# Optimization experiments

Hardware: AMD Instinct MI355X
Metric: run time of the kernel (lower is better)

## Reference

```python
import jax, jax.numpy as jnp
import numpy as np

N_NODES = 100000
N_EDGES = 1600000
N_IN = 8
N_PRE = 32
C = 128
N_LAYERS = 8


def _lin(key, fan_in, fan_out):
    kw, kb = jax.random.split(key)
    s = 1.0 / np.sqrt(fan_in).astype(np.float32)
    W = jax.random.uniform(kw, (fan_in, fan_out), minval=-s, maxval=s, dtype=jnp.float32)
    b = jax.random.uniform(kb, (fan_out,), minval=-s, maxval=s, dtype=jnp.float32)
    return W, b


def setup_inputs() -> dict:
    key = jax.random.key(0)
    ks = jax.random.split(key, 9)
    x = jax.random.normal(ks[0], (N_NODES, N_IN), dtype=jnp.float32)
    edge_index = jax.random.randint(ks[1], (2, N_EDGES), 0, N_NODES, dtype=jnp.int32)
    Wp, bp = _lin(ks[2], N_IN, N_PRE)      # preproc
    W1, b1 = _lin(ks[3], N_PRE, C)         # fc_input_1 (node_identity)
    W2, b2 = _lin(ks[4], N_PRE, C)         # fc_input_2
    Wg, bg = _lin(ks[5], C, C)             # tied GCNConv weight/bias
    Wd, bd = _lin(ks[6], 2 * C, C)         # tied dense fusion
    Wf1, bf1 = _lin(ks[7], 2 * C, C)       # final_fc1
    Wf2, bf2 = _lin(ks[8], C, 2)           # final_fc2
    return {"x": x, "edge_index": edge_index, "Wp": Wp, "bp": bp, "W1": W1, "b1": b1,
            "W2": W2, "b2": b2, "Wg": Wg, "bg": bg, "Wd": Wd, "bd": bd,
            "Wf1": Wf1, "bf1": bf1, "Wf2": Wf2, "bf2": bf2}


def _gcn(h, Wg, bg, src, dst):
    # PyG GCNConv: add self-loops, norm = deg^-1/2[src] * deg^-1/2[dst].
    # Norm factorizes, so scale at node level instead of per edge.
    hw = h @ Wg                                                  # [N, C]
    deg = jnp.zeros((N_NODES,), jnp.float32).at[dst].add(1.0) + 1.0  # +1 self-loop
    dis = jax.lax.rsqrt(deg)                                     # deg^-1/2
    hs = hw * dis[:, None]
    agg = jax.ops.segment_sum(hs[src], dst, num_segments=N_NODES)
    return (agg + hs) * dis[:, None] + bg                        # hs term = self-loop (deg^-1 * hw)


def reference(x, edge_index, Wp, bp, W1, b1, W2, b2, Wg, bg, Wd, bd, Wf1, bf1, Wf2, bf2):
    src, dst = edge_index[0], edge_index[1]
    h0 = x @ Wp + bp                       # preproc_activation = none
    ni = jax.nn.relu(h0 @ W1 + b1)         # node_identity
    h = jax.nn.relu(h0 @ W2 + b2)
    for _ in range(N_LAYERS):              # tied gnn layers; dropout is identity (inference)
        g = jax.nn.relu(_gcn(h, Wg, bg, src, dst))
        h = jax.nn.relu(jnp.concatenate([ni, g], axis=1) @ Wd + bd)
    h = jax.nn.relu(jnp.concatenate([ni, h], axis=1) @ Wf1 + bf1)
    return h @ Wf2 + bf2                   # output_activation never applied in forward
```

## Files before the change

kernel.cpp:

```cpp
#include <hip/hip_runtime.h>

#define N_NODES 100000
#define N_EDGES 1600000
#define NB 391
#define NTASK (N_NODES / 16)
#define COLPAD (N_EDGES + 7 * N_NODES + 64)

typedef unsigned short ushort_t;
typedef __attribute__((ext_vector_type(8))) short bf16x8;
typedef __attribute__((ext_vector_type(4))) float f32x4;

__device__ __forceinline__ float bf2f(unsigned short u) {
    union { unsigned u; float f; } x; x.u = ((unsigned)u) << 16; return x.f;
}
__device__ __forceinline__ unsigned short f2bf(float f) {
    union { float f; unsigned u; } x; x.f = f;
    unsigned r = x.u + 0x7fffu + ((x.u >> 16) & 1u);
    return (unsigned short)(r >> 16);
}

__global__ void k_zero(unsigned* p, int n) {
    int i = blockIdx.x * 256 + threadIdx.x;
    if (i < n) p[i] = 0u;
}

__global__ void k_filld(unsigned* p) {
    int i = blockIdx.x * 256 + threadIdx.x;
    if (i < COLPAD) p[i] = (unsigned)N_NODES;
}

__global__ void k_deg(const int* __restrict__ dst, unsigned* __restrict__ cnt) {
    int e = blockIdx.x * 256 + threadIdx.x;
    if (e < N_EDGES) atomicAdd(&cnt[dst[e]], 1u);
}

__global__ void k_dis(const unsigned* __restrict__ cnt, float* __restrict__ dis,
                      float* __restrict__ sdeg) {
    int i = blockIdx.x * 256 + threadIdx.x;
    if (i < N_NODES) {
        float d = (float)cnt[i] + 1.0f;
        float s = sqrtf(d);
        sdeg[i] = s;
        dis[i] = 1.0f / s;
    }
}

__global__ void __launch_bounds__(256) k_bsum(const unsigned* __restrict__ cnt,
                                              unsigned* __restrict__ bsum) {
    __shared__ unsigned sh[256];
    int i = blockIdx.x * 256 + threadIdx.x;
    sh[threadIdx.x] = (i < N_NODES) ? ((cnt[i] + 7u) & ~7u) : 0u;
    __syncthreads();
    for (int off = 128; off > 0; off >>= 1) {
        if (threadIdx.x < off) sh[threadIdx.x] += sh[threadIdx.x + off];
        __syncthreads();
    }
    if (threadIdx.x == 0) bsum[blockIdx.x] = sh[0];
}

__global__ void __launch_bounds__(512) k_bscan(unsigned* __restrict__ bsum) {
    __shared__ unsigned sh[512];
    int t = threadIdx.x;
    unsigned v = (t < NB) ? bsum[t] : 0u;
    sh[t] = v;
    __syncthreads();
    for (int off = 1; off < 512; off <<= 1) {
        unsigned u = (t >= off) ? sh[t - off] : 0u;
        __syncthreads();
        sh[t] += u;
        __syncthreads();
    }
    if (t < NB) bsum[t] = sh[t] - v;
}

__global__ void __launch_bounds__(256) k_apply(const unsigned* __restrict__ cnt,
                                               const unsigned* __restrict__ bsum,
                                               unsigned* __restrict__ prow,
                                               unsigned* __restrict__ cur) {
    __shared__ unsigned sh[256];
    int i = blockIdx.x * 256 + threadIdx.x;
    int t = threadIdx.x;
    unsigned v = (i < N_NODES) ? ((cnt[i] + 7u) & ~7u) : 0u;
    sh[t] = v;
    __syncthreads();
    for (int off = 1; off < 256; off <<= 1) {
        unsigned u = (t >= off) ? sh[t - off] : 0u;
        __syncthreads();
        sh[t] += u;
        __syncthreads();
    }
    if (i < N_NODES) {
        prow[i] = bsum[blockIdx.x] + sh[t] - v;
        cur[i] = 0u;
    }
    if (i == N_NODES - 1) prow[N_NODES] = bsum[blockIdx.x] + sh[t];
}

__global__ void k_fill(const int* __restrict__ src, const int* __restrict__ dst,
                       const unsigned* __restrict__ prow, unsigned* __restrict__ cur,
                       unsigned* __restrict__ colp) {
    int e = blockIdx.x * 256 + threadIdx.x;
    if (e < N_EDGES) {
        int d = dst[e];
        unsigned pos = prow[d] + atomicAdd(&cur[d], 1u);
        colp[pos] = (unsigned)src[e];
    }
}

__global__ void k_dummy(ushort_t* hdA, ushort_t* hdB) {
    int t = threadIdx.x;
    if (t < 128) hdA[(size_t)N_NODES * 128 + t] = 0;
    else hdB[(size_t)N_NODES * 128 + (t - 128)] = 0;
}

__global__ void k_tr(const float* __restrict__ Wd, const float* __restrict__ Wf1,
                     const float* __restrict__ Wg, ushort_t* __restrict__ WT) {
    const float* srcs[5] = {Wd, Wf1, Wg, Wd + 128 * 128, Wf1 + 128 * 128};
    const float* S = srcs[blockIdx.x];
    ushort_t* Dhi = WT + (size_t)(2 * blockIdx.x) * 16384;
    ushort_t* Dlo = Dhi + 16384;
    for (int i = threadIdx.x; i < 128 * 128; i += blockDim.x) {
        int n = i >> 7, k = i & 127;
        float w = S[k * 128 + n];
        unsigned short h = f2bf(w);
        Dhi[n * 128 + k] = h;
        Dlo[n * 128 + k] = f2bf(w - bf2f(h));
    }
}

__global__ void __launch_bounds__(128) k_pre1(
    const float* __restrict__ x, const float* __restrict__ Wp,
    const float* __restrict__ bp, const float* __restrict__ W1,
    const float* __restrict__ b1, const float* __restrict__ W2,
    const float* __restrict__ b2, const float* __restrict__ dis,
    ushort_t* __restrict__ ni, ushort_t* __restrict__ hd) {
    __shared__ float h0s[4][32];
    int j = threadIdx.x;
    long n0 = (long)blockIdx.x * 4;
    {
        int nn = j >> 5, c = j & 31;
        float acc = bp[c];
#pragma unroll
        for (int k = 0; k < 8; ++k)
            acc += x[(n0 + nn) * 8 + k] * Wp[k * 32 + c];
        h0s[nn][c] = acc;
    }
    __syncthreads();
    float ni_a[4], h1_a[4];
    float bb1 = b1[j], bb2 = b2[j];
#pragma unroll
    for (int m = 0; m < 4; ++m) { ni_a[m] = bb1; h1_a[m] = bb2; }
    for (int cc = 0; cc < 32; ++cc) {
        float w1 = W1[cc * 128 + j];
        float w2 = W2[cc * 128 + j];
#pragma unroll
        for (int m = 0; m < 4; ++m) {
            float h0v = h0s[m][cc];
            ni_a[m] += h0v * w1;
            h1_a[m] += h0v * w2;
        }
    }
#pragma unroll
    for (int m = 0; m < 4; ++m) {
        long node = n0 + m;
        ni[node * 128 + j] = f2bf(fmaxf(ni_a[m], 0.f));
        hd[node * 128 + j] = f2bf(fmaxf(h1_a[m], 0.f) * dis[node]);
    }
}

__device__ __forceinline__ void load_split_frags(const float* __restrict__ p,
                                                 bf16x8* ahi, bf16x8* alo) {
#pragma unroll
    for (int kc = 0; kc < 4; ++kc) {
        const float* q = p + kc * 32;
#pragma unroll
        for (int j = 0; j < 8; ++j) {
            float f = q[j];
            unsigned short h = f2bf(f);
            ahi[kc][j] = (short)h;
            alo[kc][j] = (short)f2bf(f - bf2f(h));
        }
    }
}

__device__ __forceinline__ void mfma_tiles(const bf16x8* ahi, const bf16x8* alo,
                                           const ushort_t* __restrict__ WThi,
                                           const ushort_t* __restrict__ WTlo,
                                           int r16, int q, f32x4* acc) {
#pragma unroll
    for (int t = 0; t < 8; ++t) {
        const ushort_t* bh = WThi + (t * 16 + r16) * 128 + q * 8;
        const ushort_t* bl = WTlo + (t * 16 + r16) * 128 + q * 8;
#pragma unroll
        for (int kc = 0; kc < 4; ++kc) {
            bf16x8 bhv = *(const bf16x8*)(bh + kc * 32);
            bf16x8 blv = *(const bf16x8*)(bl + kc * 32);
            acc[t] = __builtin_amdgcn_mfma_f32_16x16x32_bf16(alo[kc], bhv, acc[t], 0, 0, 0);
            acc[t] = __builtin_amdgcn_mfma_f32_16x16x32_bf16(ahi[kc], blv, acc[t], 0, 0, 0);
            acc[t] = __builtin_amdgcn_mfma_f32_16x16x32_bf16(ahi[kc], bhv, acc[t], 0, 0, 0);
        }
    }
}

__global__ void __launch_bounds__(256) gemm_bias(
    const ushort_t* __restrict__ in, const ushort_t* __restrict__ WThi,
    const ushort_t* __restrict__ WTlo, const float* __restrict__ bias,
    ushort_t* __restrict__ out) {
    int task = blockIdx.x * 4 + (threadIdx.x >> 6);
    if (task >= NTASK) return;
    int lane = threadIdx.x & 63;
    int q = lane >> 4, r16 = lane & 15;
    long base = (long)task * 16;

    bf16x8 a[4];
    const ushort_t* arow = in + (base + r16) * 128 + q * 8;
#pragma unroll
    for (int kc = 0; kc < 4; ++kc) a[kc] = *(const bf16x8*)(arow + kc * 32);

    f32x4 acc[8];
#pragma unroll
    for (int t = 0; t < 8; ++t) acc[t] = {0.f, 0.f, 0.f, 0.f};
#pragma unroll
    for (int t = 0; t < 8; ++t) {
        const ushort_t* bh = WThi + (t * 16 + r16) * 128 + q * 8;
        const ushort_t* bl = WTlo + (t * 16 + r16) * 128 + q * 8;
#pragma unroll
        for (int kc = 0; kc < 4; ++kc) {
            bf16x8 bhv = *(const bf16x8*)(bh + kc * 32);
            bf16x8 blv = *(const bf16x8*)(bl + kc * 32);
            acc[t] = __builtin_amdgcn_mfma_f32_16x16x32_bf16(a[kc], blv, acc[t], 0, 0, 0);
            acc[t] = __builtin_amdgcn_mfma_f32_16x16x32_bf16(a[kc], bhv, acc[t], 0, 0, 0);
        }
    }
#pragma unroll
    for (int t = 0; t < 8; ++t) {
        int n = t * 16 + r16;
        float bv = bias[n];
#pragma unroll
        for (int r = 0; r < 4; ++r) {
            long node = base + q * 4 + r;
            out[node * 128 + n] = f2bf(acc[t][r] + bv);
        }
    }
}

__device__ __forceinline__ void acc8(uint4 w, float* a) {
    a[0] += __uint_as_float(w.x << 16);
    a[1] += __uint_as_float(w.x & 0xffff0000u);
    a[2] += __uint_as_float(w.y << 16);
    a[3] += __uint_as_float(w.y & 0xffff0000u);
    a[4] += __uint_as_float(w.z << 16);
    a[5] += __uint_as_float(w.z & 0xffff0000u);
    a[6] += __uint_as_float(w.w << 16);
    a[7] += __uint_as_float(w.w & 0xffff0000u);
}

__device__ __forceinline__ void gather8(uint4* G, uint4 c0, uint4 c1,
                                        const uint4* __restrict__ h4, int l) {
    G[0] = h4[(long)c0.x * 16 + l];
    G[1] = h4[(long)c0.y * 16 + l];
    G[2] = h4[(long)c0.z * 16 + l];
    G[3] = h4[(long)c0.w * 16 + l];
    G[4] = h4[(long)c1.x * 16 + l];
    G[5] = h4[(long)c1.y * 16 + l];
    G[6] = h4[(long)c1.z * 16 + l];
    G[7] = h4[(long)c1.w * 16 + l];
}

__device__ __forceinline__ void accbatch(const uint4* G, float* a) {
#pragma unroll
    for (int j = 0; j < 8; ++j) acc8(G[j], a);
}

__global__ void __launch_bounds__(256, 3) k_fused(
    const unsigned* __restrict__ prow, const unsigned* __restrict__ colp,
    const ushort_t* __restrict__ hd_in,
    const ushort_t* __restrict__ hi_wg, const ushort_t* __restrict__ lo_wg,
    const float* __restrict__ bg,
    const ushort_t* __restrict__ hi_wd, const ushort_t* __restrict__ lo_wd,
    const ushort_t* __restrict__ niWd, const float* __restrict__ dis,
    ushort_t* __restrict__ hd_out) {
    __shared__ float gsh[4][16 * 132];
    int wid = threadIdx.x >> 6;
    int lane = threadIdx.x & 63;
    int task = blockIdx.x * 4 + wid;
    if (task >= NTASK) return;
    long base = (long)task * 16;
    float* gw = gsh[wid];
    const uint4* h4 = (const uint4*)hd_in;

    int g = lane >> 4;
    int l = lane & 15;

#pragma unroll 1
    for (int i = 0; i < 4; ++i) {
        int m = g * 4 + i;
        long node = base + m;
        float a[8] = {0.f, 0.f, 0.f, 0.f, 0.f, 0.f, 0.f, 0.f};
        uint4 own = h4[node * 16 + l];
        unsigned t0 = prow[node];
        int nb = (int)((prow[node + 1] - t0) >> 3);
        acc8(own, a);
        if (nb > 0) {
            const uint4* cp = (const uint4*)(colp + t0);
            uint4 cX0 = cp[0], cX1 = cp[1];
            uint4 cY0 = cp[2], cY1 = cp[3];
            cp += 4;
            uint4 GA[8], GB[8];
            gather8(GA, cX0, cX1, h4, l);
            int k = 0;
            for (; k + 2 < nb; k += 2) {
                cX0 = cp[0]; cX1 = cp[1];
                gather8(GB, cY0, cY1, h4, l);
                accbatch(GA, a);
                cY0 = cp[2]; cY1 = cp[3];
                cp += 4;
                gather8(GA, cX0, cX1, h4, l);
                accbatch(GB, a);
            }
            if (nb - k == 2) {
                gather8(GB, cY0, cY1, h4, l);
                accbatch(GA, a);
                accbatch(GB, a);
            } else {
                accbatch(GA, a);
            }
        }
        float* dstp = gw + m * 132 + 8 * l;
        *(float4*)dstp = make_float4(a[0], a[1], a[2], a[3]);
        *(float4*)(dstp + 4) = make_float4(a[4], a[5], a[6], a[7]);
    }

    int q = lane >> 4, r16 = lane & 15;
    bf16x8 ahi[4], alo[4];
    load_split_frags(gw + r16 * 132 + q * 8, ahi, alo);

    f32x4 acc[8];
#pragma unroll
    for (int t = 0; t < 8; ++t) acc[t] = {0.f, 0.f, 0.f, 0.f};
    mfma_tiles(ahi, alo, hi_wg, lo_wg, r16, q, acc);

    float sc[4];
#pragma unroll
    for (int r = 0; r < 4; ++r) sc[r] = dis[base + q * 4 + r];

#pragma unroll
    for (int t = 0; t < 8; ++t) {
        int n = t * 16 + r16;
        float bv = bg[n];
#pragma unroll
        for (int r = 0; r < 4; ++r) {
            int m = q * 4 + r;
            gw[m * 132 + n] = fmaxf(acc[t][r] * sc[r] + bv, 0.f);
        }
    }

    load_split_frags(gw + r16 * 132 + q * 8, ahi, alo);
#pragma unroll
    for (int t = 0; t < 8; ++t) acc[t] = {0.f, 0.f, 0.f, 0.f};
    mfma_tiles(ahi, alo, hi_wd, lo_wd, r16, q, acc);

#pragma unroll
    for (int t = 0; t < 8; ++t) {
        int n = t * 16 + r16;
#pragma unroll
        for (int r = 0; r < 4; ++r) {
            long node = base + q * 4 + r;
            float nv = bf2f(niWd[node * 128 + n]);
            hd_out[node * 128 + n] = f2bf(fmaxf(acc[t][r] + nv, 0.f) * sc[r]);
        }
    }
}

__global__ void __launch_bounds__(256) k_fin(
    const ushort_t* __restrict__ in, const ushort_t* __restrict__ WThi,
    const ushort_t* __restrict__ WTlo, const ushort_t* __restrict__ niWf,
    const float* __restrict__ sdeg, float* __restrict__ out) {
    int task = blockIdx.x * 4 + (threadIdx.x >> 6);
    if (task >= NTASK) return;
    int lane = threadIdx.x & 63;
    int q = lane >> 4, r16 = lane & 15;
    long base = (long)task * 16;

    bf16x8 a[4];
    const ushort_t* arow = in + (base + r16) * 128 + q * 8;
#pragma unroll
    for (int kc = 0; kc < 4; ++kc) a[kc] = *(const bf16x8*)(arow + kc * 32);

    f32x4 acc[8];
#pragma unroll
    for (int t = 0; t < 8; ++t) acc[t] = {0.f, 0.f, 0.f, 0.f};
#pragma unroll
    for (int t = 0; t < 8; ++t) {
        const ushort_t* bh = WThi + (t * 16 + r16) * 128 + q * 8;
        const ushort_t* bl = WTlo + (t * 16 + r16) * 128 + q * 8;
#pragma unroll
        for (int kc = 0; kc < 4; ++kc) {
            bf16x8 bhv = *(const bf16x8*)(bh + kc * 32);
            bf16x8 blv = *(const bf16x8*)(bl + kc * 32);
            acc[t] = __builtin_amdgcn_mfma_f32_16x16x32_bf16(a[kc], blv, acc[t], 0, 0, 0);
            acc[t] = __builtin_amdgcn_mfma_f32_16x16x32_bf16(a[kc], bhv, acc[t], 0, 0, 0);
        }
    }

    float sc[4];
#pragma unroll
    for (int r = 0; r < 4; ++r) sc[r] = sdeg[base + q * 4 + r];
#pragma unroll
    for (int t = 0; t < 8; ++t) {
        int n = t * 16 + r16;
#pragma unroll
        for (int r = 0; r < 4; ++r) {
            long node = base + q * 4 + r;
            float nv = bf2f(niWf[node * 128 + n]);
            out[node * 128 + n] = fmaxf(acc[t][r] * sc[r] + nv, 0.f);
        }
    }
}

__global__ void __launch_bounds__(256) k_fc2(const float* __restrict__ hf,
                                             const float* __restrict__ Wf2,
                                             const float* __restrict__ bf2v,
                                             float* __restrict__ out) {
    int node = blockIdx.x * 4 + (threadIdx.x >> 6);
    if (node >= N_NODES) return;
    int lane = threadIdx.x & 63;
    float2 hv = ((const float2*)hf)[(long)node * 64 + lane];
    float4 wv = *(const float4*)(Wf2 + lane * 4);
    float p0 = hv.x * wv.x + hv.y * wv.z;
    float p1 = hv.x * wv.y + hv.y * wv.w;
    for (int o = 32; o > 0; o >>= 1) {
        p0 += __shfl_down(p0, o, 64);
        p1 += __shfl_down(p1, o, 64);
    }
    if (lane == 0) {
        float2 r; r.x = p0 + bf2v[0]; r.y = p1 + bf2v[1];
        ((float2*)out)[node] = r;
    }
}

extern "C" void kernel_launch(void* const* d_in, const int* in_sizes, int n_in,
                              void* d_out, int out_size, void* d_ws, size_t ws_size,
                              hipStream_t stream) {
    const float* x    = (const float*)d_in[0];
    const int* ei     = (const int*)d_in[1];
    const float* Wp   = (const float*)d_in[2];
    const float* bp   = (const float*)d_in[3];
    const float* W1   = (const float*)d_in[4];
    const float* b1   = (const float*)d_in[5];
    const float* W2   = (const float*)d_in[6];
    const float* b2   = (const float*)d_in[7];
    const float* Wg   = (const float*)d_in[8];
    const float* bg   = (const float*)d_in[9];
    const float* Wd   = (const float*)d_in[10];
    const float* bd   = (const float*)d_in[11];
    const float* Wf1  = (const float*)d_in[12];
    const float* bf1  = (const float*)d_in[13];
    const float* Wf2  = (const float*)d_in[14];
    const float* bf2v = (const float*)d_in[15];

    char* w = (char*)d_ws;
    auto carve = [&](size_t bytes) {
        void* p = (void*)w;
        w += (bytes + 255) & ~(size_t)255;
        return p;
    };
    float* dis      = (float*)carve((size_t)N_NODES * 4);
    float* sdeg     = (float*)carve((size_t)N_NODES * 4);
    unsigned* cnt   = (unsigned*)carve((size_t)N_NODES * 4);
    unsigned* bsum  = (unsigned*)carve((size_t)NB * 4);
    unsigned* prow  = (unsigned*)carve((size_t)(N_NODES + 1) * 4);
    unsigned* colp  = (unsigned*)carve((size_t)COLPAD * 4);
    ushort_t* hdA   = (ushort_t*)carve((size_t)(N_NODES + 1) * 128 * 2);
    ushort_t* hdB   = (ushort_t*)carve((size_t)(N_NODES + 1) * 128 * 2);
    ushort_t* niB   = (ushort_t*)carve((size_t)N_NODES * 128 * 2);
    float* hf       = (float*)carve((size_t)N_NODES * 128 * 4);
    ushort_t* niWd  = (ushort_t*)carve((size_t)N_NODES * 128 * 2);
    ushort_t* niWf  = (ushort_t*)carve((size_t)N_NODES * 128 * 2);
    ushort_t* WT    = (ushort_t*)carve((size_t)10 * 16384 * 2);
    ushort_t* hi_wdtop  = WT + 0 * 16384; ushort_t* lo_wdtop  = WT + 1 * 16384;
    ushort_t* hi_wf1top = WT + 2 * 16384; ushort_t* lo_wf1top = WT + 3 * 16384;
    ushort_t* hi_wg     = WT + 4 * 16384; ushort_t* lo_wg     = WT + 5 * 16384;
    ushort_t* hi_wdbot  = WT + 6 * 16384; ushort_t* lo_wdbot  = WT + 7 * 16384;
    ushort_t* hi_wf1bot = WT + 8 * 16384; ushort_t* lo_wf1bot = WT + 9 * 16384;

    const int* srcp = ei;
    const int* dstp = ei + N_EDGES;

    const int GE = (N_EDGES + 255) / 256;
    const int GN = (N_NODES + 255) / 256;
    const int GP = (COLPAD + 255) / 256;
    const int GW = (N_NODES + 3) / 4;
    const int GG = (NTASK + 3) / 4;

    k_zero<<<GN, 256, 0, stream>>>(cnt, N_NODES);
    k_filld<<<GP, 256, 0, stream>>>(colp);
    k_deg<<<GE, 256, 0, stream>>>(dstp, cnt);
    k_dis<<<GN, 256, 0, stream>>>(cnt, dis, sdeg);
    k_bsum<<<NB, 256, 0, stream>>>(cnt, bsum);
    k_bscan<<<1, 512, 0, stream>>>(bsum);
    k_apply<<<NB, 256, 0, stream>>>(cnt, bsum, prow, cnt);
    k_fill<<<GE, 256, 0, stream>>>(srcp, dstp, prow, cnt, colp);
    k_dummy<<<1, 256, 0, stream>>>(hdA, hdB);
    k_tr<<<5, 256, 0, stream>>>(Wd, Wf1, Wg, WT);
    k_pre1<<<N_NODES / 4, 128, 0, stream>>>(x, Wp, bp, W1, b1, W2, b2, dis, niB, hdA);
    gemm_bias<<<GG, 256, 0, stream>>>(niB, hi_wdtop, lo_wdtop, bd, niWd);
    gemm_bias<<<GG, 256, 0, stream>>>(niB, hi_wf1top, lo_wf1top, bf1, niWf);
    ushort_t* hin = hdA;
    ushort_t* hout = hdB;
    for (int l = 0; l < 8; ++l) {
        k_fused<<<GG, 256, 0, stream>>>(prow, colp, hin, hi_wg, lo_wg, bg,
                                        hi_wdbot, lo_wdbot, niWd, dis, hout);
        ushort_t* tmp = hin; hin = hout; hout = tmp;
    }
    k_fin<<<GG, 256, 0, stream>>>(hin, hi_wf1bot, lo_wf1bot, niWf, sdeg, hf);
    k_fc2<<<GW, 256, 0, stream>>>(hf, Wf2, bf2v, (float*)d_out);
}
```

Before: 1.776 ms.

## Sort CSR neighbor lists, fuse ni GEMMs, raise fused-kernel occupancy

Adds a per-node insertion sort of CSR column indices after the fill step, so gathers in each of the 8 GCN layers visit source rows in ascending order and get better cache and DRAM locality. The two bias GEMMs on the node-identity features become one kernel that loads the A operand once and writes both outputs. The launch bound of the fused layer kernel goes from 3 to 4 blocks per SM, which may force register spilling. The sort adds a one-time serial cost per node, about 16 elements per node on average.

Result: slower. 1.886 ms (+6.2%).

```diff
diff --git a/kernel.cpp b/kernel.cpp
--- a/kernel.cpp
+++ b/kernel.cpp
@@ -107,6 +107,19 @@
     }
 }
 
+__global__ void __launch_bounds__(256) k_sort(const unsigned* __restrict__ prow,
+                                              unsigned* __restrict__ colp) {
+    int i = blockIdx.x * 256 + threadIdx.x;
+    if (i >= N_NODES) return;
+    unsigned b = prow[i], e = prow[i + 1];
+    for (unsigned j = b + 1; j < e; ++j) {
+        unsigned v = colp[j];
+        unsigned k = j;
+        while (k > b && colp[k - 1] > v) { colp[k] = colp[k - 1]; --k; }
+        colp[k] = v;
+    }
+}
+
 __global__ void k_dummy(ushort_t* hdA, ushort_t* hdB) {
     int t = threadIdx.x;
     if (t < 128) hdA[(size_t)N_NODES * 128 + t] = 0;
@@ -202,10 +215,12 @@
     }
 }
 
-__global__ void __launch_bounds__(256) gemm_bias(
-    const ushort_t* __restrict__ in, const ushort_t* __restrict__ WThi,
-    const ushort_t* __restrict__ WTlo, const float* __restrict__ bias,
-    ushort_t* __restrict__ out) {
+__global__ void __launch_bounds__(256) k_niw(
+    const ushort_t* __restrict__ in,
+    const ushort_t* __restrict__ hiA, const ushort_t* __restrict__ loA,
+    const float* __restrict__ biasA, ushort_t* __restrict__ outA,
+    const ushort_t* __restrict__ hiB, const ushort_t* __restrict__ loB,
+    const float* __restrict__ biasB, ushort_t* __restrict__ outB) {
     int task = blockIdx.x * 4 + (threadIdx.x >> 6);
     if (task >= NTASK) return;
     int lane = threadIdx.x & 63;
@@ -217,29 +232,32 @@
 #pragma unroll
     for (int kc = 0; kc < 4; ++kc) a[kc] = *(const bf16x8*)(arow + kc * 32);
 
-    f32x4 acc[8];
-#pragma unroll
-    for (int t = 0; t < 8; ++t) acc[t] = {0.f, 0.f, 0.f, 0.f};
-#pragma unroll
-    for (int t = 0; t < 8; ++t) {
-        const ushort_t* bh = WThi + (t * 16 + r16) * 128 + q * 8;
-        const ushort_t* bl = WTlo + (t * 16 + r16) * 128 + q * 8;
+    f32x4 accA[8], accB[8];
+#pragma unroll
+    for (int t = 0; t < 8; ++t) { accA[t] = {0.f, 0.f, 0.f, 0.f}; accB[t] = {0.f, 0.f, 0.f, 0.f}; }
+#pragma unroll
+    for (int t = 0; t < 8; ++t) {
+        const ushort_t* bhA = hiA + (t * 16 + r16) * 128 + q * 8;
+        const ushort_t* blA = loA + (t * 16 + r16) * 128 + q * 8;
+        const ushort_t* bhB = hiB + (t * 16 + r16) * 128 + q * 8;
+        const ushort_t* blB = loB + (t * 16 + r16) * 128 + q * 8;
 #pragma unroll
         for (int kc = 0; kc < 4; ++kc) {
-            bf16x8 bhv = *(const bf16x8*)(bh + kc * 32);
-            bf16x8 blv = *(const bf16x8*)(bl + kc * 32);
-            acc[t] = __builtin_amdgcn_mfma_f32_16x16x32_bf16(a[kc], blv, acc[t], 0, 0, 0);
-            acc[t] = __builtin_amdgcn_mfma_f32_16x16x32_bf16(a[kc], bhv, acc[t], 0, 0, 0);
+            accA[t] = __builtin_amdgcn_mfma_f32_16x16x32_bf16(a[kc], *(const bf16x8*)(blA + kc * 32), accA[t], 0, 0, 0);
+            accA[t] = __builtin_amdgcn_mfma_f32_16x16x32_bf16(a[kc], *(const bf16x8*)(bhA + kc * 32), accA[t], 0, 0, 0);
+            accB[t] = __builtin_amdgcn_mfma_f32_16x16x32_bf16(a[kc], *(const bf16x8*)(blB + kc * 32), accB[t], 0, 0, 0);
+            accB[t] = __builtin_amdgcn_mfma_f32_16x16x32_bf16(a[kc], *(const bf16x8*)(bhB + kc * 32), accB[t], 0, 0, 0);
         }
     }
 #pragma unroll
     for (int t = 0; t < 8; ++t) {
         int n = t * 16 + r16;
-        float bv = bias[n];
+        float bvA = biasA[n], bvB = biasB[n];
 #pragma unroll
         for (int r = 0; r < 4; ++r) {
             long node = base + q * 4 + r;
-            out[node * 128 + n] = f2bf(acc[t][r] + bv);
+            outA[node * 128 + n] = f2bf(accA[t][r] + bvA);
+            outB[node * 128 + n] = f2bf(accB[t][r] + bvB);
         }
     }
 }
@@ -272,7 +290,7 @@
     for (int j = 0; j < 8; ++j) acc8(G[j], a);
 }
 
-__global__ void __launch_bounds__(256, 3) k_fused(
+__global__ void __launch_bounds__(256, 4) k_fused(
     const unsigned* __restrict__ prow, const unsigned* __restrict__ colp,
     const ushort_t* __restrict__ hd_in,
     const ushort_t* __restrict__ hi_wg, const ushort_t* __restrict__ lo_wg,
@@ -501,11 +519,12 @@
     k_bscan<<<1, 512, 0, stream>>>(bsum);
     k_apply<<<NB, 256, 0, stream>>>(cnt, bsum, prow, cnt);
     k_fill<<<GE, 256, 0, stream>>>(srcp, dstp, prow, cnt, colp);
+    k_sort<<<GN, 256, 0, stream>>>(prow, colp);
     k_dummy<<<1, 256, 0, stream>>>(hdA, hdB);
     k_tr<<<5, 256, 0, stream>>>(Wd, Wf1, Wg, WT);
     k_pre1<<<N_NODES / 4, 128, 0, stream>>>(x, Wp, bp, W1, b1, W2, b2, dis, niB, hdA);
-    gemm_bias<<<GG, 256, 0, stream>>>(niB, hi_wdtop, lo_wdtop, bd, niWd);
-    gemm_bias<<<GG, 256, 0, stream>>>(niB, hi_wf1top, lo_wf1top, bf1, niWf);
+    k_niw<<<GG, 256, 0, stream>>>(niB, hi_wdtop, lo_wdtop, bd, niWd,
+                                  hi_wf1top, lo_wf1top, bf1, niWf);
     ushort_t* hin = hdA;
     ushort_t* hout = hdB;
     for (int l = 0; l < 8; ++l) {
```
